# Optimization experiments

Hardware: AMD Instinct MI355X
Metric: run time of the kernel (lower is better)

The kernel has to match this reference:

```python
import jax, jax.numpy as jnp
import numpy as np

B, T, D = 8, 2048, 128


def setup_inputs() -> dict:
    key = jax.random.key(0)
    kq, kk, kv = jax.random.split(key, 3)
    q = jax.random.normal(kq, (B, T, D), dtype=jnp.float32)
    k = jax.random.normal(kk, (B, T, D), dtype=jnp.float32)
    v = jax.random.normal(kv, (B, T, D), dtype=jnp.float32)
    # causal mask, broadcast over batch; 0 -> masked
    mask = jnp.tril(jnp.ones((T, T), dtype=jnp.int32))[None, :, :]
    mode = jnp.float32(0.5)  # learnable scalar parameter (init 0.5)
    return {"q": q, "k": k, "v": v, "mask": mask, "mode": mode}


def reference(q, k, v, mask, mode):
    scale = D ** (-0.5)
    # meson score: -(Q K^T) * scale
    meson = -jnp.einsum("btd,bsd->bts", q, k) * scale
    # baryon score: Q against K with feature dim rolled by 1
    k_perm = jnp.roll(k, shift=1, axis=-1)
    baryon = jnp.einsum("btd,bsd->bts", q, k_perm) * scale
    alpha = jax.nn.sigmoid(mode)
    attn = alpha * meson + (1.0 - alpha) * baryon
    attn = jnp.where(mask == 0, -jnp.inf, attn)
    attn = jax.nn.softmax(attn, axis=-1)
    return jnp.einsum("bts,bsd->btd", attn, v)
```

## Files before the change

### kernel.cpp

```cpp
#include <hip/hip_runtime.h>
#include <hip/hip_bf16.h>
#include <cstdint>
#include <cstddef>


typedef __attribute__((ext_vector_type(8))) short short8;
typedef __attribute__((ext_vector_type(4))) float f32x4;

#define T_DIM 2048
#define D_DIM 128
#define B_DIM 8
#define MAXSEG 4

__device__ __forceinline__ unsigned short f2bf(float f) {
  unsigned u = __builtin_bit_cast(unsigned, f);
  u += 0x7FFFu + ((u >> 16) & 1u);
  return (unsigned short)(u >> 16);
}
__device__ __forceinline__ float bf2f(unsigned short u) {
  return __uint_as_float(((unsigned)u) << 16);
}
__device__ __forceinline__ void gload_lds16(const void* g, void* l) {
  __builtin_amdgcn_global_load_lds(
      (const __attribute__((address_space(1))) unsigned int*)g,
      (__attribute__((address_space(3))) unsigned int*)l, 16, 0, 0);
}

__global__ void prep_kq(const float* __restrict__ k, const float* __restrict__ q,
                        const float* __restrict__ modep,
                        unsigned short* __restrict__ kbf, unsigned short* __restrict__ qbf) {
  int i = blockIdx.x * 256 + threadIdx.x;
  float4 ka = ((const float4*)k)[2 * i], kb = ((const float4*)k)[2 * i + 1];
  short8 ko = { (short)f2bf(ka.x), (short)f2bf(ka.y), (short)f2bf(ka.z), (short)f2bf(ka.w),
                (short)f2bf(kb.x), (short)f2bf(kb.y), (short)f2bf(kb.z), (short)f2bf(kb.w) };
  ((short8*)kbf)[i] = ko;
  int row = i >> 4, c8 = i & 15;
  const float* qr = q + (size_t)row * D_DIM;
  float e[9];
  float4 f0 = *(const float4*)(qr + c8 * 8);
  float4 f1 = *(const float4*)(qr + c8 * 8 + 4);
  e[0] = f0.x; e[1] = f0.y; e[2] = f0.z; e[3] = f0.w;
  e[4] = f1.x; e[5] = f1.y; e[6] = f1.z; e[7] = f1.w;
  e[8] = qr[(c8 * 8 + 8) & 127];
  const float alpha = 1.f / (1.f + __expf(-modep[0]));
  const float scale = 0.08838834764831845f;
  const float ca = -alpha * scale, cb = (1.f - alpha) * scale;
  short8 o;
#pragma unroll
  for (int j = 0; j < 8; ++j) o[j] = (short)f2bf(ca * e[j] + cb * e[j + 1]);
  ((short8*)qbf)[i] = o;
}

__global__ void tv_kernel(const float* __restrict__ v, unsigned short* __restrict__ vt) {
  __shared__ float tile[64][65];
  const int b = blockIdx.z, d0 = blockIdx.y * 64, s0 = blockIdx.x * 64;
  const int tid = threadIdx.x;
#pragma unroll
  for (int u = 0; u < 4; ++u) {
    int flat = u * 256 + tid; int r = flat >> 4, c4 = flat & 15;
    float4 f = *(const float4*)(v + ((size_t)b * T_DIM + s0 + r) * D_DIM + d0 + c4 * 4);
    tile[r][c4 * 4 + 0] = f.x; tile[r][c4 * 4 + 1] = f.y;
    tile[r][c4 * 4 + 2] = f.z; tile[r][c4 * 4 + 3] = f.w;
  }
  __syncthreads();
#pragma unroll
  for (int u = 0; u < 4; ++u) {
    int flat = u * 256 + tid; int dr = flat >> 4, sq = flat & 15;
    ushort4 o = { f2bf(tile[sq * 4 + 0][dr]), f2bf(tile[sq * 4 + 1][dr]),
                  f2bf(tile[sq * 4 + 2][dr]), f2bf(tile[sq * 4 + 3][dr]) };
    *(ushort4*)(vt + ((size_t)b * D_DIM + d0 + dr) * T_DIM + s0 + sq * 4) = o;
  }
}

__global__ __launch_bounds__(256, 2) void attn_kernel(
    const unsigned short* __restrict__ qbf, const unsigned short* __restrict__ kbf,
    const unsigned short* __restrict__ vt, float* __restrict__ out,
    unsigned short* __restrict__ po, float* __restrict__ ml, int segt)
{
  __shared__ uint4 smem4[5120];
  char* smem = (char*)smem4;
  const int tid = threadIdx.x;
  const int w = tid >> 6, lane = tid & 63;
  const int t16 = lane & 15, g = lane >> 4;
  const int b = blockIdx.x;
  const int qc = blockIdx.y, seg = blockIdx.z;
  const int nt = 2 * qc + 2;
  const int nseg = (nt + segt - 1) / segt;
  if (seg >= nseg) return;
  const int t0 = seg * segt;
  const int t1 = min(nt, t0 + segt);
  const int qb = qc * 128 + w * 32;
  const int tdiag = qb >> 6;

  char* pw = smem + 65536 + w * 4096;
  const unsigned short* kbase = kbf + (size_t)b * T_DIM * D_DIM;
  const unsigned short* vbase = vt + (size_t)b * D_DIM * T_DIM;

  short8 qf[2][4];
#pragma unroll
  for (int mt = 0; mt < 2; ++mt) {
    const unsigned short* qr = qbf + ((size_t)b * T_DIM + qb + mt * 16 + t16) * D_DIM + g * 8;
#pragma unroll
    for (int dd = 0; dd < 4; ++dd) qf[mt][dd] = *(const short8*)(qr + dd * 32);
  }

  f32x4 acc[2][8];
#pragma unroll
  for (int mt = 0; mt < 2; ++mt)
#pragma unroll
    for (int dt = 0; dt < 8; ++dt) acc[mt][dt] = (f32x4){0.f, 0.f, 0.f, 0.f};
  float mrun[2][4], lrun[2][4];
#pragma unroll
  for (int mt = 0; mt < 2; ++mt)
#pragma unroll
    for (int r = 0; r < 4; ++r) { mrun[mt][r] = -1e30f; lrun[mt][r] = 0.f; }

  auto stage = [&](int cur, int kt) {
    const int kv0 = kt * 64;
    char* kb = smem + cur * 16384;
    char* vb = smem + 32768 + cur * 16384;
#pragma unroll
    for (int u = 0; u < 4; ++u) {
      int s_loc = w * 16 + u * 4 + (lane >> 4);
      int slot = (lane & 15) ^ (s_loc & 7);
      gload_lds16(kbase + (size_t)(kv0 + s_loc) * D_DIM + slot * 8,
                  kb + w * 4096 + u * 1024);
    }
    const int vslot = (lane & 7) ^ ((lane >> 3) & 7);
#pragma unroll
    for (int u = 0; u < 4; ++u) {
      int d_loc = w * 32 + u * 8 + (lane >> 3);
      gload_lds16(vbase + (size_t)d_loc * T_DIM + kv0 + vslot * 8,
                  vb + w * 4096 + u * 1024);
    }
  };

  stage(0, t0);
  __syncthreads();
  int cur = 0;

  for (int kt = t0; kt < t1; ++kt) {
    if (kt + 1 < t1) stage(cur ^ 1, kt + 1);

    if (kt <= tdiag) {
      const int kv0 = kt * 64;
      char* kb = smem + cur * 16384;
      char* vb = smem + 32768 + cur * 16384;

      f32x4 sj[2][4];
#pragma unroll
      for (int jt = 0; jt < 4; ++jt) {
        int s = jt * 16 + t16;
        int rb = s * 256, swz = (s & 7) << 4;
        f32x4 s0 = (f32x4){0.f, 0.f, 0.f, 0.f};
        f32x4 s1 = (f32x4){0.f, 0.f, 0.f, 0.f};
#pragma unroll
        for (int dd = 0; dd < 4; ++dd) {
          short8 kf = *(const short8*)(kb + ((rb + dd * 64 + g * 16) ^ swz));
          s0 = __builtin_amdgcn_mfma_f32_16x16x32_bf16(qf[0][dd], kf, s0, 0, 0, 0);
          s1 = __builtin_amdgcn_mfma_f32_16x16x32_bf16(qf[1][dd], kf, s1, 0, 0, 0);
        }
        sj[0][jt] = s0; sj[1][jt] = s1;
      }

      const bool needmask = (kt == tdiag);
#pragma unroll
      for (int mt = 0; mt < 2; ++mt) {
        if (needmask) {
#pragma unroll
          for (int jt = 0; jt < 4; ++jt) {
            int sg = kv0 + jt * 16 + t16;
#pragma unroll
            for (int r = 0; r < 4; ++r) {
              int tg = qb + mt * 16 + 4 * g + r;
              if (sg > tg) sj[mt][jt][r] = -1e30f;
            }
          }
        }
        float tm[4];
#pragma unroll
        for (int r = 0; r < 4; ++r)
          tm[r] = fmaxf(fmaxf(sj[mt][0][r], sj[mt][1][r]), fmaxf(sj[mt][2][r], sj[mt][3][r]));
#pragma unroll
        for (int r = 0; r < 4; ++r) {
          tm[r] = fmaxf(tm[r], __shfl_xor(tm[r], 1));
          tm[r] = fmaxf(tm[r], __shfl_xor(tm[r], 2));
          tm[r] = fmaxf(tm[r], __shfl_xor(tm[r], 4));
          tm[r] = fmaxf(tm[r], __shfl_xor(tm[r], 8));
        }
        float corr[4], rs[4];
#pragma unroll
        for (int r = 0; r < 4; ++r) {
          float mnew = fmaxf(mrun[mt][r], tm[r]);
          corr[r] = __expf(mrun[mt][r] - mnew);
          mrun[mt][r] = mnew;
          rs[r] = 0.f;
        }
#pragma unroll
        for (int jt = 0; jt < 4; ++jt)
#pragma unroll
          for (int r = 0; r < 4; ++r) {
            float p = __expf(sj[mt][jt][r] - mrun[mt][r]);
            sj[mt][jt][r] = p;
            rs[r] += p;
          }
#pragma unroll
        for (int r = 0; r < 4; ++r) {
          rs[r] += __shfl_xor(rs[r], 1);
          rs[r] += __shfl_xor(rs[r], 2);
          rs[r] += __shfl_xor(rs[r], 4);
          rs[r] += __shfl_xor(rs[r], 8);
          lrun[mt][r] = lrun[mt][r] * corr[r] + rs[r];
        }
#pragma unroll
        for (int dt = 0; dt < 8; ++dt)
#pragma unroll
          for (int r = 0; r < 4; ++r) acc[mt][dt][r] *= corr[r];
        char* pb = pw + mt * 2048;
#pragma unroll
        for (int jt = 0; jt < 4; ++jt)
#pragma unroll
          for (int r = 0; r < 4; ++r) {
            int rloc = 4 * g + r;
            *(unsigned short*)(pb + rloc * 128 + ((2 * (jt * 16 + t16)) ^ ((rloc & 7) << 4))) =
                f2bf(sj[mt][jt][r]);
          }
      }

#pragma unroll
      for (int k0 = 0; k0 < 2; ++k0) {
        short8 pf0 = *(const short8*)(pw + t16 * 128 + ((k0 * 64 + g * 16) ^ ((t16 & 7) << 4)));
        short8 pf1 = *(const short8*)(pw + 2048 + t16 * 128 + ((k0 * 64 + g * 16) ^ ((t16 & 7) << 4)));
#pragma unroll
        for (int dt = 0; dt < 8; ++dt) {
          int d = dt * 16 + t16;
          short8 vf = *(const short8*)(vb + d * 128 + (((k0 * 4 + g) << 4) ^ ((d & 7) << 4)));
          acc[0][dt] = __builtin_amdgcn_mfma_f32_16x16x32_bf16(pf0, vf, acc[0][dt], 0, 0, 0);
          acc[1][dt] = __builtin_amdgcn_mfma_f32_16x16x32_bf16(pf1, vf, acc[1][dt], 0, 0, 0);
        }
      }
    }

    __syncthreads();
    cur ^= 1;
  }

  if (nseg == 1) {
#pragma unroll
    for (int mt = 0; mt < 2; ++mt)
#pragma unroll
      for (int r = 0; r < 4; ++r) {
        float inv = 1.0f / lrun[mt][r];
#pragma unroll
        for (int dt = 0; dt < 8; ++dt)
          out[((size_t)b * T_DIM + qc * 128 + w * 32 + mt * 16 + 4 * g + r) * D_DIM + dt * 16 + t16] =
              acc[mt][dt][r] * inv;
      }
  } else {
    const int slot = (b * 16 + qc) * MAXSEG + seg;
    unsigned short* pob = po + (size_t)slot * 16384;
#pragma unroll
    for (int mt = 0; mt < 2; ++mt)
#pragma unroll
      for (int r = 0; r < 4; ++r) {
        int rb = w * 32 + mt * 16 + 4 * g + r;
#pragma unroll
        for (int dt = 0; dt < 8; ++dt)
          pob[rb * 128 + dt * 16 + t16] = f2bf(acc[mt][dt][r]);
      }
    if (t16 == 0) {
#pragma unroll
      for (int mt = 0; mt < 2; ++mt)
#pragma unroll
        for (int r = 0; r < 4; ++r) {
          int rb = w * 32 + mt * 16 + 4 * g + r;
          ml[(size_t)slot * 256 + rb] = mrun[mt][r];
          ml[(size_t)slot * 256 + 128 + rb] = lrun[mt][r];
        }
    }
  }
}

__global__ __launch_bounds__(256) void combine_kernel(
    const unsigned short* __restrict__ po, const float* __restrict__ ml,
    float* __restrict__ out, int segt)
{
  const int tid = threadIdx.x;
  const int b = blockIdx.x;
  const int qc = 4 + (int)blockIdx.y;
  const int nt = 2 * qc + 2;
  const int nseg = (nt + segt - 1) / segt;
  const int slot0 = (b * 16 + qc) * MAXSEG;

  __shared__ float wgt[128][MAXSEG];
  if (tid < 128) {
    float M = -1e30f;
    for (int s = 0; s < nseg; ++s)
      M = fmaxf(M, ml[(size_t)(slot0 + s) * 256 + tid]);
    float L = 0.f;
    for (int s = 0; s < nseg; ++s) {
      float e = __expf(ml[(size_t)(slot0 + s) * 256 + tid] - M);
      wgt[tid][s] = e;
      L += e * ml[(size_t)(slot0 + s) * 256 + 128 + tid];
    }
    float invL = 1.f / L;
    for (int s = 0; s < nseg; ++s) wgt[tid][s] *= invL;
  }
  __syncthreads();

#pragma unroll
  for (int it = 0; it < 8; ++it) {
    int vid = it * 256 + tid;
    int r = vid >> 4, ch = vid & 15;
    float o[8] = {0.f, 0.f, 0.f, 0.f, 0.f, 0.f, 0.f, 0.f};
    for (int s = 0; s < nseg; ++s) {
      short8 pv = *(const short8*)(po + (size_t)(slot0 + s) * 16384 + r * 128 + ch * 8);
      float ws = wgt[r][s];
#pragma unroll
      for (int j = 0; j < 8; ++j) o[j] += ws * bf2f((unsigned short)pv[j]);
    }
    float* dst = out + ((size_t)b * T_DIM + qc * 128 + r) * D_DIM + ch * 8;
    *(float4*)(dst) = (float4){o[0], o[1], o[2], o[3]};
    *(float4*)(dst + 4) = (float4){o[4], o[5], o[6], o[7]};
  }
}

extern "C" void kernel_launch(void* const* d_in, const int* in_sizes, int n_in,
                              void* d_out, int out_size, void* d_ws, size_t ws_size,
                              hipStream_t stream) {
  const float* q = (const float*)d_in[0];
  const float* k = (const float*)d_in[1];
  const float* v = (const float*)d_in[2];
  const float* mode = (const float*)d_in[4];
  float* out = (float*)d_out;

  char* ws = (char*)d_ws;
  unsigned short* kbf = (unsigned short*)(ws);
  unsigned short* vtb = (unsigned short*)(ws + 4194304);
  unsigned short* qbf = (unsigned short*)(ws + 8388608);
  unsigned short* po  = (unsigned short*)(ws + 12582912);
  float*          ml  = (float*)(ws + 29360128);

  const bool split = ws_size >= 29884416ULL;
  const int segt = split ? 8 : 32;

  prep_kq<<<1024, 256, 0, stream>>>(k, q, mode, kbf, qbf);
  tv_kernel<<<dim3(T_DIM / 64, D_DIM / 64, B_DIM), 256, 0, stream>>>(v, vtb);
  attn_kernel<<<dim3(B_DIM, 16, split ? MAXSEG : 1), 256, 0, stream>>>(
      qbf, kbf, vtb, out, po, ml, segt);
  if (split)
    combine_kernel<<<dim3(B_DIM, 12), 256, 0, stream>>>(po, ml, out, segt);
}
```

Baseline: 63.38 us.

## Fuse prep kernels and shrink attention blocks to 64 query rows

Merges the K/Q conversion and the V transpose into one prep kernel, removing one launch and the separate V read pass. The attention kernel now uses 2 waves and 64 query rows per block, doubling the grid and dropping the wasted half-tile diagonal work. It also replaces double-buffered K/V staging with single-buffered loads fenced by syncthreads, which cuts LDS use but gives up load/compute overlap. Each wave now handles its two 16-row groups sequentially through one P buffer.

Measured after the change: 58.60 us. -7.5%, faster.

```diff
diff --git a/kernel.cpp b/kernel.cpp
--- a/kernel.cpp
+++ b/kernel.cpp
@@ -26,73 +26,79 @@
       (__attribute__((address_space(3))) unsigned int*)l, 16, 0, 0);
 }
 
-__global__ void prep_kq(const float* __restrict__ k, const float* __restrict__ q,
-                        const float* __restrict__ modep,
-                        unsigned short* __restrict__ kbf, unsigned short* __restrict__ qbf) {
-  int i = blockIdx.x * 256 + threadIdx.x;
-  float4 ka = ((const float4*)k)[2 * i], kb = ((const float4*)k)[2 * i + 1];
-  short8 ko = { (short)f2bf(ka.x), (short)f2bf(ka.y), (short)f2bf(ka.z), (short)f2bf(ka.w),
-                (short)f2bf(kb.x), (short)f2bf(kb.y), (short)f2bf(kb.z), (short)f2bf(kb.w) };
-  ((short8*)kbf)[i] = ko;
-  int row = i >> 4, c8 = i & 15;
-  const float* qr = q + (size_t)row * D_DIM;
-  float e[9];
-  float4 f0 = *(const float4*)(qr + c8 * 8);
-  float4 f1 = *(const float4*)(qr + c8 * 8 + 4);
-  e[0] = f0.x; e[1] = f0.y; e[2] = f0.z; e[3] = f0.w;
-  e[4] = f1.x; e[5] = f1.y; e[6] = f1.z; e[7] = f1.w;
-  e[8] = qr[(c8 * 8 + 8) & 127];
+__global__ __launch_bounds__(256) void prep_all(
+    const float* __restrict__ q, const float* __restrict__ k, const float* __restrict__ v,
+    const float* __restrict__ modep,
+    unsigned short* __restrict__ qbf, unsigned short* __restrict__ kbf,
+    unsigned short* __restrict__ vt)
+{
+  __shared__ unsigned short tile[64 * 136];
+  const int b = blockIdx.x, s0 = blockIdx.y * 64;
+  const int tid = threadIdx.x;
   const float alpha = 1.f / (1.f + __expf(-modep[0]));
   const float scale = 0.08838834764831845f;
   const float ca = -alpha * scale, cb = (1.f - alpha) * scale;
-  short8 o;
-#pragma unroll
-  for (int j = 0; j < 8; ++j) o[j] = (short)f2bf(ca * e[j] + cb * e[j + 1]);
-  ((short8*)qbf)[i] = o;
-}
-
-__global__ void tv_kernel(const float* __restrict__ v, unsigned short* __restrict__ vt) {
-  __shared__ float tile[64][65];
-  const int b = blockIdx.z, d0 = blockIdx.y * 64, s0 = blockIdx.x * 64;
-  const int tid = threadIdx.x;
+
 #pragma unroll
   for (int u = 0; u < 4; ++u) {
-    int flat = u * 256 + tid; int r = flat >> 4, c4 = flat & 15;
-    float4 f = *(const float4*)(v + ((size_t)b * T_DIM + s0 + r) * D_DIM + d0 + c4 * 4);
-    tile[r][c4 * 4 + 0] = f.x; tile[r][c4 * 4 + 1] = f.y;
-    tile[r][c4 * 4 + 2] = f.z; tile[r][c4 * 4 + 3] = f.w;
+    int c = u * 256 + tid;
+    int r = c >> 4, c8 = c & 15;
+    size_t row = (size_t)b * T_DIM + s0 + r;
+    float4 ka = *(const float4*)(k + row * D_DIM + c8 * 8);
+    float4 kb2 = *(const float4*)(k + row * D_DIM + c8 * 8 + 4);
+    short8 ko = { (short)f2bf(ka.x), (short)f2bf(ka.y), (short)f2bf(ka.z), (short)f2bf(ka.w),
+                  (short)f2bf(kb2.x), (short)f2bf(kb2.y), (short)f2bf(kb2.z), (short)f2bf(kb2.w) };
+    *(short8*)(kbf + row * D_DIM + c8 * 8) = ko;
+    const float* qr = q + row * D_DIM;
+    float e[9];
+    float4 f0 = *(const float4*)(qr + c8 * 8);
+    float4 f1 = *(const float4*)(qr + c8 * 8 + 4);
+    e[0] = f0.x; e[1] = f0.y; e[2] = f0.z; e[3] = f0.w;
+    e[4] = f1.x; e[5] = f1.y; e[6] = f1.z; e[7] = f1.w;
+    e[8] = qr[(c8 * 8 + 8) & 127];
+    short8 qo;
+#pragma unroll
+    for (int j = 0; j < 8; ++j) qo[j] = (short)f2bf(ca * e[j] + cb * e[j + 1]);
+    *(short8*)(qbf + row * D_DIM + c8 * 8) = qo;
+    float4 va = *(const float4*)(v + row * D_DIM + c8 * 8);
+    float4 vb2 = *(const float4*)(v + row * D_DIM + c8 * 8 + 4);
+    short8 vo = { (short)f2bf(va.x), (short)f2bf(va.y), (short)f2bf(va.z), (short)f2bf(va.w),
+                  (short)f2bf(vb2.x), (short)f2bf(vb2.y), (short)f2bf(vb2.z), (short)f2bf(vb2.w) };
+    *(short8*)(tile + r * 136 + c8 * 8) = vo;
   }
   __syncthreads();
 #pragma unroll
-  for (int u = 0; u < 4; ++u) {
-    int flat = u * 256 + tid; int dr = flat >> 4, sq = flat & 15;
-    ushort4 o = { f2bf(tile[sq * 4 + 0][dr]), f2bf(tile[sq * 4 + 1][dr]),
-                  f2bf(tile[sq * 4 + 2][dr]), f2bf(tile[sq * 4 + 3][dr]) };
-    *(ushort4*)(vt + ((size_t)b * D_DIM + d0 + dr) * T_DIM + s0 + sq * 4) = o;
-  }
-}
-
-__global__ __launch_bounds__(256, 2) void attn_kernel(
+  for (int u = 0; u < 8; ++u) {
+    int c = u * 256 + tid;
+    int d = c >> 4, sq = c & 15;
+    ushort4 o = { tile[(sq * 4 + 0) * 136 + d], tile[(sq * 4 + 1) * 136 + d],
+                  tile[(sq * 4 + 2) * 136 + d], tile[(sq * 4 + 3) * 136 + d] };
+    *(ushort4*)(vt + ((size_t)b * D_DIM + d) * T_DIM + s0 + sq * 4) = o;
+  }
+}
+
+__global__ __launch_bounds__(128, 2) void attn_kernel(
     const unsigned short* __restrict__ qbf, const unsigned short* __restrict__ kbf,
     const unsigned short* __restrict__ vt, float* __restrict__ out,
     unsigned short* __restrict__ po, float* __restrict__ ml, int segt)
 {
-  __shared__ uint4 smem4[5120];
+  __shared__ uint4 smem4[2304];
   char* smem = (char*)smem4;
   const int tid = threadIdx.x;
   const int w = tid >> 6, lane = tid & 63;
   const int t16 = lane & 15, g = lane >> 4;
   const int b = blockIdx.x;
   const int qc = blockIdx.y, seg = blockIdx.z;
-  const int nt = 2 * qc + 2;
+  const int nt = qc + 1;
   const int nseg = (nt + segt - 1) / segt;
   if (seg >= nseg) return;
   const int t0 = seg * segt;
   const int t1 = min(nt, t0 + segt);
-  const int qb = qc * 128 + w * 32;
-  const int tdiag = qb >> 6;
-
-  char* pw = smem + 65536 + w * 4096;
+  const int qb = qc * 64 + w * 32;
+
+  char* kb = smem;
+  char* vb = smem + 16384;
+  char* pw = smem + 32768 + w * 2048;
   const unsigned short* kbase = kbf + (size_t)b * T_DIM * D_DIM;
   const unsigned short* vbase = vt + (size_t)b * D_DIM * T_DIM;
 
@@ -115,134 +121,115 @@
 #pragma unroll
     for (int r = 0; r < 4; ++r) { mrun[mt][r] = -1e30f; lrun[mt][r] = 0.f; }
 
-  auto stage = [&](int cur, int kt) {
+  for (int kt = t0; kt < t1; ++kt) {
     const int kv0 = kt * 64;
-    char* kb = smem + cur * 16384;
-    char* vb = smem + 32768 + cur * 16384;
-#pragma unroll
-    for (int u = 0; u < 4; ++u) {
-      int s_loc = w * 16 + u * 4 + (lane >> 4);
+    __syncthreads();
+#pragma unroll
+    for (int u = 0; u < 8; ++u) {
+      int s_loc = w * 32 + u * 4 + (lane >> 4);
       int slot = (lane & 15) ^ (s_loc & 7);
       gload_lds16(kbase + (size_t)(kv0 + s_loc) * D_DIM + slot * 8,
-                  kb + w * 4096 + u * 1024);
-    }
-    const int vslot = (lane & 7) ^ ((lane >> 3) & 7);
-#pragma unroll
-    for (int u = 0; u < 4; ++u) {
-      int d_loc = w * 32 + u * 8 + (lane >> 3);
+                  kb + w * 8192 + u * 1024);
+    }
+#pragma unroll
+    for (int u = 0; u < 8; ++u) {
+      int d_loc = w * 64 + u * 8 + (lane >> 3);
+      int vslot = (lane & 7) ^ (d_loc & 7);
       gload_lds16(vbase + (size_t)d_loc * T_DIM + kv0 + vslot * 8,
-                  vb + w * 4096 + u * 1024);
-    }
-  };
-
-  stage(0, t0);
-  __syncthreads();
-  int cur = 0;
-
-  for (int kt = t0; kt < t1; ++kt) {
-    if (kt + 1 < t1) stage(cur ^ 1, kt + 1);
-
-    if (kt <= tdiag) {
-      const int kv0 = kt * 64;
-      char* kb = smem + cur * 16384;
-      char* vb = smem + 32768 + cur * 16384;
-
-      f32x4 sj[2][4];
-#pragma unroll
-      for (int jt = 0; jt < 4; ++jt) {
-        int s = jt * 16 + t16;
-        int rb = s * 256, swz = (s & 7) << 4;
-        f32x4 s0 = (f32x4){0.f, 0.f, 0.f, 0.f};
-        f32x4 s1 = (f32x4){0.f, 0.f, 0.f, 0.f};
-#pragma unroll
-        for (int dd = 0; dd < 4; ++dd) {
-          short8 kf = *(const short8*)(kb + ((rb + dd * 64 + g * 16) ^ swz));
-          s0 = __builtin_amdgcn_mfma_f32_16x16x32_bf16(qf[0][dd], kf, s0, 0, 0, 0);
-          s1 = __builtin_amdgcn_mfma_f32_16x16x32_bf16(qf[1][dd], kf, s1, 0, 0, 0);
-        }
-        sj[0][jt] = s0; sj[1][jt] = s1;
-      }
-
-      const bool needmask = (kt == tdiag);
-#pragma unroll
-      for (int mt = 0; mt < 2; ++mt) {
-        if (needmask) {
-#pragma unroll
-          for (int jt = 0; jt < 4; ++jt) {
-            int sg = kv0 + jt * 16 + t16;
-#pragma unroll
-            for (int r = 0; r < 4; ++r) {
-              int tg = qb + mt * 16 + 4 * g + r;
-              if (sg > tg) sj[mt][jt][r] = -1e30f;
-            }
+                  vb + w * 8192 + u * 1024);
+    }
+    __syncthreads();
+
+    f32x4 sj[2][4];
+#pragma unroll
+    for (int jt = 0; jt < 4; ++jt) {
+      int s = jt * 16 + t16;
+      int rb = s * 256, swz = (s & 7) << 4;
+      f32x4 s0 = (f32x4){0.f, 0.f, 0.f, 0.f};
+      f32x4 s1 = (f32x4){0.f, 0.f, 0.f, 0.f};
+#pragma unroll
+      for (int dd = 0; dd < 4; ++dd) {
+        short8 kf = *(const short8*)(kb + ((rb + dd * 64 + g * 16) ^ swz));
+        s0 = __builtin_amdgcn_mfma_f32_16x16x32_bf16(qf[0][dd], kf, s0, 0, 0, 0);
+        s1 = __builtin_amdgcn_mfma_f32_16x16x32_bf16(qf[1][dd], kf, s1, 0, 0, 0);
+      }
+      sj[0][jt] = s0; sj[1][jt] = s1;
+    }
+
+    const bool needmask = (kt == nt - 1);
+#pragma unroll
+    for (int mt = 0; mt < 2; ++mt) {
+      if (needmask) {
+#pragma unroll
+        for (int jt = 0; jt < 4; ++jt) {
+          int sg = kv0 + jt * 16 + t16;
+#pragma unroll
+          for (int r = 0; r < 4; ++r) {
+            int tg = qb + mt * 16 + 4 * g + r;
+            if (sg > tg) sj[mt][jt][r] = -1e30f;
           }
         }
-        float tm[4];
-#pragma unroll
-        for (int r = 0; r < 4; ++r)
-          tm[r] = fmaxf(fmaxf(sj[mt][0][r], sj[mt][1][r]), fmaxf(sj[mt][2][r], sj[mt][3][r]));
+      }
+      float tm[4];
+#pragma unroll
+      for (int r = 0; r < 4; ++r)
+        tm[r] = fmaxf(fmaxf(sj[mt][0][r], sj[mt][1][r]), fmaxf(sj[mt][2][r], sj[mt][3][r]));
+#pragma unroll
+      for (int r = 0; r < 4; ++r) {
+        tm[r] = fmaxf(tm[r], __shfl_xor(tm[r], 1));
+        tm[r] = fmaxf(tm[r], __shfl_xor(tm[r], 2));
+        tm[r] = fmaxf(tm[r], __shfl_xor(tm[r], 4));
+        tm[r] = fmaxf(tm[r], __shfl_xor(tm[r], 8));
+      }
+      float corr[4], rs[4];
+#pragma unroll
+      for (int r = 0; r < 4; ++r) {
+        float mnew = fmaxf(mrun[mt][r], tm[r]);
+        corr[r] = __expf(mrun[mt][r] - mnew);
+        mrun[mt][r] = mnew;
+        rs[r] = 0.f;
+      }
+#pragma unroll
+      for (int jt = 0; jt < 4; ++jt)
 #pragma unroll
         for (int r = 0; r < 4; ++r) {
-          tm[r] = fmaxf(tm[r], __shfl_xor(tm[r], 1));
-          tm[r] = fmaxf(tm[r], __shfl_xor(tm[r], 2));
-          tm[r] = fmaxf(tm[r], __shfl_xor(tm[r], 4));
-          tm[r] = fmaxf(tm[r], __shfl_xor(tm[r], 8));
-        }
-        float corr[4], rs[4];
+          float p = __expf(sj[mt][jt][r] - mrun[mt][r]);
+          sj[mt][jt][r] = p;
+          rs[r] += p;
+        }
+#pragma unroll
+      for (int r = 0; r < 4; ++r) {
+        rs[r] += __shfl_xor(rs[r], 1);
+        rs[r] += __shfl_xor(rs[r], 2);
+        rs[r] += __shfl_xor(rs[r], 4);
+        rs[r] += __shfl_xor(rs[r], 8);
+        lrun[mt][r] = lrun[mt][r] * corr[r] + rs[r];
+      }
+#pragma unroll
+      for (int dt = 0; dt < 8; ++dt)
+#pragma unroll
+        for (int r = 0; r < 4; ++r) acc[mt][dt][r] *= corr[r];
+
+#pragma unroll
+      for (int jt = 0; jt < 4; ++jt)
 #pragma unroll
         for (int r = 0; r < 4; ++r) {
-          float mnew = fmaxf(mrun[mt][r], tm[r]);
-          corr[r] = __expf(mrun[mt][r] - mnew);
-          mrun[mt][r] = mnew;
-          rs[r] = 0.f;
-        }
-#pragma unroll
-        for (int jt = 0; jt < 4; ++jt)
-#pragma unroll
-          for (int r = 0; r < 4; ++r) {
-            float p = __expf(sj[mt][jt][r] - mrun[mt][r]);
-            sj[mt][jt][r] = p;
-            rs[r] += p;
-          }
-#pragma unroll
-        for (int r = 0; r < 4; ++r) {
-          rs[r] += __shfl_xor(rs[r], 1);
-          rs[r] += __shfl_xor(rs[r], 2);
-          rs[r] += __shfl_xor(rs[r], 4);
-          rs[r] += __shfl_xor(rs[r], 8);
-          lrun[mt][r] = lrun[mt][r] * corr[r] + rs[r];
-        }
-#pragma unroll
-        for (int dt = 0; dt < 8; ++dt)
-#pragma unroll
-          for (int r = 0; r < 4; ++r) acc[mt][dt][r] *= corr[r];
-        char* pb = pw + mt * 2048;
-#pragma unroll
-        for (int jt = 0; jt < 4; ++jt)
-#pragma unroll
-          for (int r = 0; r < 4; ++r) {
-            int rloc = 4 * g + r;
-            *(unsigned short*)(pb + rloc * 128 + ((2 * (jt * 16 + t16)) ^ ((rloc & 7) << 4))) =
-                f2bf(sj[mt][jt][r]);
-          }
-      }
+          int rloc = 4 * g + r;
+          *(unsigned short*)(pw + rloc * 128 + ((2 * (jt * 16 + t16)) ^ ((rloc & 7) << 4))) =
+              f2bf(sj[mt][jt][r]);
+        }
 
 #pragma unroll
       for (int k0 = 0; k0 < 2; ++k0) {
-        short8 pf0 = *(const short8*)(pw + t16 * 128 + ((k0 * 64 + g * 16) ^ ((t16 & 7) << 4)));
-        short8 pf1 = *(const short8*)(pw + 2048 + t16 * 128 + ((k0 * 64 + g * 16) ^ ((t16 & 7) << 4)));
+        short8 pf = *(const short8*)(pw + t16 * 128 + ((k0 * 64 + g * 16) ^ ((t16 & 7) << 4)));
 #pragma unroll
         for (int dt = 0; dt < 8; ++dt) {
           int d = dt * 16 + t16;
           short8 vf = *(const short8*)(vb + d * 128 + (((k0 * 4 + g) << 4) ^ ((d & 7) << 4)));
-          acc[0][dt] = __builtin_amdgcn_mfma_f32_16x16x32_bf16(pf0, vf, acc[0][dt], 0, 0, 0);
-          acc[1][dt] = __builtin_amdgcn_mfma_f32_16x16x32_bf16(pf1, vf, acc[1][dt], 0, 0, 0);
-        }
-      }
-    }
-
-    __syncthreads();
-    cur ^= 1;
+          acc[mt][dt] = __builtin_amdgcn_mfma_f32_16x16x32_bf16(pf, vf, acc[mt][dt], 0, 0, 0);
+        }
+      }
+    }
   }
 
   if (nseg == 1) {
@@ -253,12 +240,12 @@
         float inv = 1.0f / lrun[mt][r];
 #pragma unroll
         for (int dt = 0; dt < 8; ++dt)
-          out[((size_t)b * T_DIM + qc * 128 + w * 32 + mt * 16 + 4 * g + r) * D_DIM + dt * 16 + t16] =
+          out[((size_t)b * T_DIM + qb + mt * 16 + 4 * g + r) * D_DIM + dt * 16 + t16] =
               acc[mt][dt][r] * inv;
       }
   } else {
-    const int slot = (b * 16 + qc) * MAXSEG + seg;
-    unsigned short* pob = po + (size_t)slot * 16384;
+    const int slot = (b * 32 + qc) * MAXSEG + seg;
+    unsigned short* pob = po + (size_t)slot * 8192;
 #pragma unroll
     for (int mt = 0; mt < 2; ++mt)
 #pragma unroll
@@ -274,8 +261,8 @@
 #pragma unroll
         for (int r = 0; r < 4; ++r) {
           int rb = w * 32 + mt * 16 + 4 * g + r;
-          ml[(size_t)slot * 256 + rb] = mrun[mt][r];
-          ml[(size_t)slot * 256 + 128 + rb] = lrun[mt][r];
+          ml[(size_t)slot * 128 + rb] = mrun[mt][r];
+          ml[(size_t)slot * 128 + 64 + rb] = lrun[mt][r];
         }
     }
   }
@@ -287,21 +274,21 @@
 {
   const int tid = threadIdx.x;
   const int b = blockIdx.x;
-  const int qc = 4 + (int)blockIdx.y;
-  const int nt = 2 * qc + 2;
+  const int qc = segt + (int)blockIdx.y;
+  const int nt = qc + 1;
   const int nseg = (nt + segt - 1) / segt;
-  const int slot0 = (b * 16 + qc) * MAXSEG;
-
-  __shared__ float wgt[128][MAXSEG];
-  if (tid < 128) {
+  const int slot0 = (b * 32 + qc) * MAXSEG;
+
+  __shared__ float wgt[64][MAXSEG];
+  if (tid < 64) {
     float M = -1e30f;
     for (int s = 0; s < nseg; ++s)
-      M = fmaxf(M, ml[(size_t)(slot0 + s) * 256 + tid]);
+      M = fmaxf(M, ml[(size_t)(slot0 + s) * 128 + tid]);
     float L = 0.f;
     for (int s = 0; s < nseg; ++s) {
-      float e = __expf(ml[(size_t)(slot0 + s) * 256 + tid] - M);
+      float e = __expf(ml[(size_t)(slot0 + s) * 128 + tid] - M);
       wgt[tid][s] = e;
-      L += e * ml[(size_t)(slot0 + s) * 256 + 128 + tid];
+      L += e * ml[(size_t)(slot0 + s) * 128 + 64 + tid];
     }
     float invL = 1.f / L;
     for (int s = 0; s < nseg; ++s) wgt[tid][s] *= invL;
@@ -309,17 +296,17 @@
   __syncthreads();
 
 #pragma unroll
-  for (int it = 0; it < 8; ++it) {
+  for (int it = 0; it < 4; ++it) {
     int vid = it * 256 + tid;
     int r = vid >> 4, ch = vid & 15;
     float o[8] = {0.f, 0.f, 0.f, 0.f, 0.f, 0.f, 0.f, 0.f};
     for (int s = 0; s < nseg; ++s) {
-      short8 pv = *(const short8*)(po + (size_t)(slot0 + s) * 16384 + r * 128 + ch * 8);
+      short8 pv = *(const short8*)(po + (size_t)(slot0 + s) * 8192 + r * 128 + ch * 8);
       float ws = wgt[r][s];
 #pragma unroll
       for (int j = 0; j < 8; ++j) o[j] += ws * bf2f((unsigned short)pv[j]);
     }
-    float* dst = out + ((size_t)b * T_DIM + qc * 128 + r) * D_DIM + ch * 8;
+    float* dst = out + ((size_t)b * T_DIM + qc * 64 + r) * D_DIM + ch * 8;
     *(float4*)(dst) = (float4){o[0], o[1], o[2], o[3]};
     *(float4*)(dst + 4) = (float4){o[4], o[5], o[6], o[7]};
   }
@@ -335,19 +322,18 @@
   float* out = (float*)d_out;
 
   char* ws = (char*)d_ws;
-  unsigned short* kbf = (unsigned short*)(ws);
-  unsigned short* vtb = (unsigned short*)(ws + 4194304);
-  unsigned short* qbf = (unsigned short*)(ws + 8388608);
+  unsigned short* qbf = (unsigned short*)(ws);
+  unsigned short* kbf = (unsigned short*)(ws + 4194304);
+  unsigned short* vtb = (unsigned short*)(ws + 8388608);
   unsigned short* po  = (unsigned short*)(ws + 12582912);
   float*          ml  = (float*)(ws + 29360128);
 
   const bool split = ws_size >= 29884416ULL;
   const int segt = split ? 8 : 32;
 
-  prep_kq<<<1024, 256, 0, stream>>>(k, q, mode, kbf, qbf);
-  tv_kernel<<<dim3(T_DIM / 64, D_DIM / 64, B_DIM), 256, 0, stream>>>(v, vtb);
-  attn_kernel<<<dim3(B_DIM, 16, split ? MAXSEG : 1), 256, 0, stream>>>(
+  prep_all<<<dim3(B_DIM, T_DIM / 64), 256, 0, stream>>>(q, k, v, mode, qbf, kbf, vtb);
+  attn_kernel<<<dim3(B_DIM, 32, split ? MAXSEG : 1), 128, 0, stream>>>(
       qbf, kbf, vtb, out, po, ml, segt);
   if (split)
-    combine_kernel<<<dim3(B_DIM, 12), 256, 0, stream>>>(po, ml, out, segt);
-}
+    combine_kernel<<<dim3(B_DIM, 24), 256, 0, stream>>>(po, ml, out, segt);
+}
```
